# Optimization experiments

Hardware: AMD Instinct MI355X
Metric: run time of the kernel (lower is better)

## Reference

```python
import jax, jax.numpy as jnp
import numpy as np

LN_EPS = 1e-5  # torch.nn.LayerNorm default


def setup_inputs() -> dict:
    key = jax.random.key(0)
    ks = jax.random.split(key, 6)
    b, e, c, h, w, m = 4, 16, 256, 32, 64, 1024
    return {
        "x": jax.random.normal(ks[0], (b, e, c, h, w), dtype=jnp.float32),
        "ln_w": jnp.ones((c, h, w), dtype=jnp.float32),
        "ln_b": jnp.zeros((c, h, w), dtype=jnp.float32),
        "w_in": jax.random.normal(ks[1], (c, m), dtype=jnp.float32) * (1.0 / np.sqrt(c)),
        "b_in": jax.random.normal(ks[2], (m,), dtype=jnp.float32) * 0.01,
        "w_out": jax.random.normal(ks[3], (m, c), dtype=jnp.float32) * (1.0 / np.sqrt(m)),
        "b_out": jax.random.normal(ks[4], (c,), dtype=jnp.float32) * 0.01,
        "gamma": jnp.full((c,), 1e-6, dtype=jnp.float32),
    }


def reference(x, ln_w, ln_b, w_in, b_in, w_out, b_out, gamma):
    # LayerNorm over the last 3 dims (c, h, w) with affine params of shape (c, h, w)
    mu = jnp.mean(x, axis=(-3, -2, -1), keepdims=True)
    var = jnp.var(x, axis=(-3, -2, -1), keepdims=True)  # biased, matches torch
    y = (x - mu) * jax.lax.rsqrt(var + LN_EPS)
    y = y * ln_w + ln_b  # broadcast (c,h,w) over (b,e,...)

    # b e c h w -> b e h w c
    y = jnp.moveaxis(y, 2, -1)
    t = jax.nn.gelu(y @ w_in + b_in, approximate=False)  # torch GELU is exact erf
    t = (t @ w_out + b_out) * gamma  # layer scale on channel dim

    # b e h w c -> b e c h w, residual add
    return x + jnp.moveaxis(t, -1, 2)
```

## Files before the change

### kernel.cpp

```cpp
#include <hip/hip_runtime.h>
#include <math.h>

#define NS 64
#define CD 256
#define HW 2048
#define MD 1024
#define SAMPLE (CD * HW)
#define LN_EPS 1e-5f

#define PB 128
#define MC 32
#define NCH (MD / MC)

typedef float f32x4 __attribute__((ext_vector_type(4)));
typedef long i64;

__device__ __forceinline__ int swz(int p) {
  int k = (p ^ (p >> 2)) & 15;
  return ((k & 7) << 4) | (k & 8);
}

__device__ __forceinline__ void gl_lds16(const unsigned char* g, unsigned char* l) {
  __builtin_amdgcn_global_load_lds(
      (const __attribute__((address_space(1))) unsigned char*)g,
      (__attribute__((address_space(3))) unsigned char*)l, 16, 0, 0);
}

__global__ __launch_bounds__(256) void k_prep(const float* __restrict__ w_in,
                                              const float* __restrict__ w_out,
                                              unsigned char* __restrict__ w_in8p,
                                              unsigned char* __restrict__ w_out8p) {
  int id = blockIdx.x * 256 + threadIdx.x;
  if (id < 65536) {
    int i = id;
    int f = i >> 7, l = (i >> 1) & 63, j0 = (i & 1) * 4;
    int m = (f >> 3) * 16 + (l & 15);
    int c0 = (f & 7) * 32 + (l >> 4) * 8 + j0;
    float a = w_in[(size_t)(c0 + 0) * MD + m];
    float b = w_in[(size_t)(c0 + 1) * MD + m];
    float c = w_in[(size_t)(c0 + 2) * MD + m];
    float d = w_in[(size_t)(c0 + 3) * MD + m];
    int r = __builtin_amdgcn_cvt_pk_fp8_f32(a, b, 0, false);
    r = __builtin_amdgcn_cvt_pk_fp8_f32(c, d, r, true);
    ((int*)w_in8p)[i] = r;
  } else {
    int i = id - 65536;
    int g = i >> 7, l = (i >> 1) & 63, j0 = (i & 1) * 4;
    int c = (g & 15) * 16 + (l & 15);
    int m0 = (g >> 4) * 32 + (l >> 4) * 8 + j0;
    float a = w_out[(size_t)(m0 + 0) * CD + c];
    float b = w_out[(size_t)(m0 + 1) * CD + c];
    float cc = w_out[(size_t)(m0 + 2) * CD + c];
    float d = w_out[(size_t)(m0 + 3) * CD + c];
    int r = __builtin_amdgcn_cvt_pk_fp8_f32(a, b, 0, false);
    r = __builtin_amdgcn_cvt_pk_fp8_f32(cc, d, r, true);
    ((int*)w_out8p)[i] = r;
  }
}

__global__ __launch_bounds__(256) void k_stats1(const float* __restrict__ x,
                                                double* __restrict__ partial) {
  int s = blockIdx.x >> 3, sl = blockIdx.x & 7;
  const float4* p = (const float4*)(x + (size_t)s * SAMPLE + (size_t)sl * 65536);
  double sum = 0.0, ssq = 0.0;
  for (int i = 0; i < 64; ++i) {
    float4 v = p[i * 256 + threadIdx.x];
    sum += (double)v.x + (double)v.y + (double)v.z + (double)v.w;
    ssq += (double)v.x * v.x + (double)v.y * v.y + (double)v.z * v.z + (double)v.w * v.w;
  }
  for (int off = 32; off; off >>= 1) {
    sum += __shfl_down(sum, off);
    ssq += __shfl_down(ssq, off);
  }
  __shared__ double red[4][2];
  int wv = threadIdx.x >> 6, ln = threadIdx.x & 63;
  if (ln == 0) { red[wv][0] = sum; red[wv][1] = ssq; }
  __syncthreads();
  if (threadIdx.x == 0) {
    for (int i = 1; i < 4; ++i) { sum += red[i][0]; ssq += red[i][1]; }
    partial[blockIdx.x * 2] = sum;
    partial[blockIdx.x * 2 + 1] = ssq;
  }
}

__global__ void k_stats2(const double* __restrict__ partial, float* __restrict__ stats) {
  int s = threadIdx.x;
  double sum = 0.0, ssq = 0.0;
  for (int i = 0; i < 8; ++i) {
    sum += partial[(s * 8 + i) * 2];
    ssq += partial[(s * 8 + i) * 2 + 1];
  }
  double mean = sum / (double)SAMPLE;
  double var = ssq / (double)SAMPLE - mean * mean;
  stats[s * 2] = (float)mean;
  stats[s * 2 + 1] = (float)(1.0 / sqrt(var + (double)LN_EPS));
}

__global__ __launch_bounds__(512, 4) void k_fused(
    const float* __restrict__ x, const float* __restrict__ ln_w, const float* __restrict__ ln_b,
    const float* __restrict__ b_in, const float* __restrict__ b_out, const float* __restrict__ gamma,
    const unsigned char* __restrict__ w_in8p, const unsigned char* __restrict__ w_out8p,
    const float* __restrict__ stats, float* __restrict__ out) {
  __shared__ unsigned char Ysh[128 * 256];
  __shared__ unsigned char Wsh1[2][16 * 512];
  __shared__ unsigned char Wsh2[2][16 * 512];

  const int tid = threadIdx.x;
  const int lane = tid & 63, l15 = lane & 15, l4 = lane >> 4;
  const int wv = tid >> 6;
  const int s = blockIdx.x >> 4;
  const int p0 = (blockIdx.x & 15) * PB;
  const float mu = stats[s * 2], rstd = stats[s * 2 + 1];
  const float a_ln = rstd, c_ln = -mu * rstd;
  const size_t xbase = (size_t)s * SAMPLE;

  gl_lds16(w_in8p + wv * 1024 + lane * 16, &Wsh1[0][wv * 1024]);
  gl_lds16(w_out8p + wv * 1024 + lane * 16, &Wsh2[0][wv * 1024]);

  #pragma unroll
  for (int it = 0; it < 4; ++it) {
    int bid = it * 512 + tid;
    int c0 = (bid >> 5) * 4, pp = (bid & 31) * 4;
    float yv[4][4];
    #pragma unroll
    for (int i = 0; i < 4; ++i) {
      size_t off = (size_t)(c0 + i) * HW + p0 + pp;
      float4 xv = *(const float4*)(x + xbase + off);
      float4 lw = *(const float4*)(ln_w + off);
      float4 lb = *(const float4*)(ln_b + off);
      yv[i][0] = fmaf(fmaf(xv.x, a_ln, c_ln), lw.x, lb.x);
      yv[i][1] = fmaf(fmaf(xv.y, a_ln, c_ln), lw.y, lb.y);
      yv[i][2] = fmaf(fmaf(xv.z, a_ln, c_ln), lw.z, lb.z);
      yv[i][3] = fmaf(fmaf(xv.w, a_ln, c_ln), lw.w, lb.w);
    }
    #pragma unroll
    for (int j = 0; j < 4; ++j) {
      int p = pp + j;
      int r = __builtin_amdgcn_cvt_pk_fp8_f32(yv[0][j], yv[1][j], 0, false);
      r = __builtin_amdgcn_cvt_pk_fp8_f32(yv[2][j], yv[3][j], r, true);
      *(int*)&Ysh[p * 256 + (c0 ^ swz(p))] = r;
    }
  }

  const int strip = wv * 16;
  const int pY = strip + l15;
  const int sY = swz(pY);
  f32x4 acc2[16] = {};

  __syncthreads();

  i64 breg[8];
  #pragma unroll
  for (int kk = 0; kk < 8; ++kk)
    breg[kk] = *(const i64*)&Ysh[pY * 256 + ((kk * 32 + l4 * 8) ^ sY)];

  for (int ch = 0; ch < NCH; ++ch) {
    const int b = ch & 1;

    if (ch + 1 < NCH) {
      const size_t co = (size_t)(ch + 1) * 8192;
      gl_lds16(w_in8p + co + wv * 1024 + lane * 16, &Wsh1[b ^ 1][wv * 1024]);
      gl_lds16(w_out8p + co + wv * 1024 + lane * 16, &Wsh2[b ^ 1][wv * 1024]);
    }

    const unsigned char* W1 = Wsh1[b];
    f32x4 acc1[2] = {};
    #pragma unroll
    for (int kk = 0; kk < 8; ++kk) {
      i64 a0 = *(const i64*)&W1[(kk)*512 + lane * 8];
      i64 a1 = *(const i64*)&W1[(8 + kk) * 512 + lane * 8];
      acc1[0] = __builtin_amdgcn_mfma_f32_16x16x32_fp8_fp8(a0, breg[kk], acc1[0], 0, 0, 0);
      acc1[1] = __builtin_amdgcn_mfma_f32_16x16x32_fp8_fp8(a1, breg[kk], acc1[1], 0, 0, 0);
    }

    int pk0, pk1;
    #pragma unroll
    for (int mt = 0; mt < 2; ++mt) {
      const float4 bi = *(const float4*)&b_in[ch * 32 + mt * 16 + l4 * 4];
      float g[4];
      #pragma unroll
      for (int r = 0; r < 4; ++r) {
        float t = acc1[mt][r] + ((const float*)&bi)[r];
        g[r] = t * __builtin_amdgcn_rcpf(1.0f + __expf(-1.702f * t));
      }
      int pk = __builtin_amdgcn_cvt_pk_fp8_f32(g[0], g[1], 0, false);
      pk = __builtin_amdgcn_cvt_pk_fp8_f32(g[2], g[3], pk, true);
      if (mt == 0) pk0 = pk; else pk1 = pk;
    }

    {
      const int sl = l15 + 32 * (l4 & 1);
      int v0a = __shfl(pk0, sl), v0b = __shfl(pk1, sl);
      int v1a = __shfl(pk0, sl + 16), v1b = __shfl(pk1, sl + 16);
      int vlo = (l4 & 2) ? v0b : v0a;
      int vhi = (l4 & 2) ? v1b : v1a;
      i64 a2 = (i64)((((unsigned long long)(unsigned)vhi) << 32) | (unsigned)vlo);

      const unsigned char* W2 = Wsh2[b];
      #pragma unroll
      for (int ct = 0; ct < 16; ++ct) {
        i64 b2 = *(const i64*)&W2[ct * 512 + lane * 8];
        acc2[ct] = __builtin_amdgcn_mfma_f32_16x16x32_fp8_fp8(a2, b2, acc2[ct], 0, 0, 0);
      }
    }

    __syncthreads();
  }

  #pragma unroll
  for (int ct = 0; ct < 16; ++ct) {
    int cc = ct * 16 + l15;
    float gm = gamma[cc], bo = b_out[cc];
    int p = p0 + strip + l4 * 4;
    size_t off = xbase + (size_t)cc * HW + p;
    float4 xv = *(const float4*)(x + off);
    float4 o;
    #pragma unroll
    for (int r = 0; r < 4; ++r)
      ((float*)&o)[r] = ((const float*)&xv)[r] + gm * (acc2[ct][r] + bo);
    *(float4*)(out + off) = o;
  }
}

extern "C" void kernel_launch(void* const* d_in, const int* in_sizes, int n_in,
                              void* d_out, int out_size, void* d_ws, size_t ws_size,
                              hipStream_t stream) {
  const float* x = (const float*)d_in[0];
  const float* ln_w = (const float*)d_in[1];
  const float* ln_b = (const float*)d_in[2];
  const float* w_in = (const float*)d_in[3];
  const float* b_in = (const float*)d_in[4];
  const float* w_out = (const float*)d_in[5];
  const float* b_out = (const float*)d_in[6];
  const float* gamma = (const float*)d_in[7];
  float* out = (float*)d_out;

  char* ws = (char*)d_ws;
  unsigned char* w_in8p = (unsigned char*)ws;
  unsigned char* w_out8p = (unsigned char*)(ws + 262144);
  double* partial = (double*)(ws + 524288);
  float* stats = (float*)(ws + 524288 + 8192);

  k_prep<<<512, 256, 0, stream>>>(w_in, w_out, w_in8p, w_out8p);
  k_stats1<<<512, 256, 0, stream>>>(x, partial);
  k_stats2<<<1, 64, 0, stream>>>(partial, stats);

  k_fused<<<1024, 512, 0, stream>>>(x, ln_w, ln_b, b_in, b_out, gamma,
                                    w_in8p, w_out8p, stats, out);
}
```

Before: 196.0 us.

## Skew second GEMM one chunk behind to overlap GELU with MFMA

Restructures the chunk loop so each iteration runs the second GEMM for the previous chunk's GELU output together with the first GEMM for the current chunk. This gives the scheduler independent MFMA work while GELU, fp8 packing and the lane shuffles are in flight. The w_out staging becomes triple-buffered in dynamic shared memory so the lagging reads stay valid, and s_setprio raises wave priority around the MFMA section. LDS per block grows from 64 KB to 72 KB, and a drain step after the loop handles the last chunk.

```diff
diff --git a/kernel.cpp b/kernel.cpp
--- a/kernel.cpp
+++ b/kernel.cpp
@@ -101,9 +101,10 @@
     const float* __restrict__ b_in, const float* __restrict__ b_out, const float* __restrict__ gamma,
     const unsigned char* __restrict__ w_in8p, const unsigned char* __restrict__ w_out8p,
     const float* __restrict__ stats, float* __restrict__ out) {
-  __shared__ unsigned char Ysh[128 * 256];
-  __shared__ unsigned char Wsh1[2][16 * 512];
-  __shared__ unsigned char Wsh2[2][16 * 512];
+  extern __shared__ unsigned char smem[];
+  unsigned char* Ysh = smem;
+  unsigned char* Wsh1 = smem + 32768;
+  unsigned char* Wsh2 = smem + 49152;
 
   const int tid = threadIdx.x;
   const int lane = tid & 63, l15 = lane & 15, l4 = lane >> 4;
@@ -114,8 +115,8 @@
   const float a_ln = rstd, c_ln = -mu * rstd;
   const size_t xbase = (size_t)s * SAMPLE;
 
-  gl_lds16(w_in8p + wv * 1024 + lane * 16, &Wsh1[0][wv * 1024]);
-  gl_lds16(w_out8p + wv * 1024 + lane * 16, &Wsh2[0][wv * 1024]);
+  gl_lds16(w_in8p + wv * 1024 + lane * 16, Wsh1 + wv * 1024);
+  gl_lds16(w_out8p + wv * 1024 + lane * 16, Wsh2 + wv * 1024);
 
   #pragma unroll
   for (int it = 0; it < 4; ++it) {
@@ -154,16 +155,30 @@
   for (int kk = 0; kk < 8; ++kk)
     breg[kk] = *(const i64*)&Ysh[pY * 256 + ((kk * 32 + l4 * 8) ^ sY)];
 
+  i64 a2_prev = 0;
+
   for (int ch = 0; ch < NCH; ++ch) {
-    const int b = ch & 1;
+    if (ch) __syncthreads();
 
     if (ch + 1 < NCH) {
       const size_t co = (size_t)(ch + 1) * 8192;
-      gl_lds16(w_in8p + co + wv * 1024 + lane * 16, &Wsh1[b ^ 1][wv * 1024]);
-      gl_lds16(w_out8p + co + wv * 1024 + lane * 16, &Wsh2[b ^ 1][wv * 1024]);
-    }
-
-    const unsigned char* W1 = Wsh1[b];
+      gl_lds16(w_in8p + co + wv * 1024 + lane * 16,
+               Wsh1 + ((ch + 1) & 1) * 8192 + wv * 1024);
+      gl_lds16(w_out8p + co + wv * 1024 + lane * 16,
+               Wsh2 + ((ch + 1) % 3) * 8192 + wv * 1024);
+    }
+
+    __builtin_amdgcn_s_setprio(1);
+    if (ch) {
+      const unsigned char* W2 = Wsh2 + ((ch - 1) % 3) * 8192;
+      #pragma unroll
+      for (int ct = 0; ct < 16; ++ct) {
+        i64 b2 = *(const i64*)&W2[ct * 512 + lane * 8];
+        acc2[ct] = __builtin_amdgcn_mfma_f32_16x16x32_fp8_fp8(a2_prev, b2, acc2[ct], 0, 0, 0);
+      }
+    }
+
+    const unsigned char* W1 = Wsh1 + (ch & 1) * 8192;
     f32x4 acc1[2] = {};
     #pragma unroll
     for (int kk = 0; kk < 8; ++kk) {
@@ -172,6 +187,7 @@
       acc1[0] = __builtin_amdgcn_mfma_f32_16x16x32_fp8_fp8(a0, breg[kk], acc1[0], 0, 0, 0);
       acc1[1] = __builtin_amdgcn_mfma_f32_16x16x32_fp8_fp8(a1, breg[kk], acc1[1], 0, 0, 0);
     }
+    __builtin_amdgcn_s_setprio(0);
 
     int pk0, pk1;
     #pragma unroll
@@ -194,17 +210,17 @@
       int v1a = __shfl(pk0, sl + 16), v1b = __shfl(pk1, sl + 16);
       int vlo = (l4 & 2) ? v0b : v0a;
       int vhi = (l4 & 2) ? v1b : v1a;
-      i64 a2 = (i64)((((unsigned long long)(unsigned)vhi) << 32) | (unsigned)vlo);
-
-      const unsigned char* W2 = Wsh2[b];
-      #pragma unroll
-      for (int ct = 0; ct < 16; ++ct) {
-        i64 b2 = *(const i64*)&W2[ct * 512 + lane * 8];
-        acc2[ct] = __builtin_amdgcn_mfma_f32_16x16x32_fp8_fp8(a2, b2, acc2[ct], 0, 0, 0);
-      }
-    }
-
-    __syncthreads();
+      a2_prev = (i64)((((unsigned long long)(unsigned)vhi) << 32) | (unsigned)vlo);
+    }
+  }
+
+  {
+    const unsigned char* W2 = Wsh2 + ((NCH - 1) % 3) * 8192;
+    #pragma unroll
+    for (int ct = 0; ct < 16; ++ct) {
+      i64 b2 = *(const i64*)&W2[ct * 512 + lane * 8];
+      acc2[ct] = __builtin_amdgcn_mfma_f32_16x16x32_fp8_fp8(a2_prev, b2, acc2[ct], 0, 0, 0);
+    }
   }
 
   #pragma unroll
@@ -245,6 +261,9 @@
   k_stats1<<<512, 256, 0, stream>>>(x, partial);
   k_stats2<<<1, 64, 0, stream>>>(partial, stats);
 
-  k_fused<<<1024, 512, 0, stream>>>(x, ln_w, ln_b, b_in, b_out, gamma,
-                                    w_in8p, w_out8p, stats, out);
-}
+  const int lds_bytes = 32768 + 16384 + 24576;
+  hipFuncSetAttribute((const void*)k_fused, hipFuncAttributeMaxDynamicSharedMemorySize,
+                      lds_bytes);
+  k_fused<<<1024, 512, lds_bytes, stream>>>(x, ln_w, ln_b, b_in, b_out, gamma,
+                                            w_in8p, w_out8p, stats, out);
+}
```

After: 182.9 us. 6.7% less time.

## Halve pixel tile, split waves over M/C halves, software-pipeline the two GEMMs

Applied to the files above, without the earlier changes.

The pixel block is halved to 64 and the grid doubled. Pairs of waves now split the hidden chunk and output channels, which halves the accumulator registers and raises the launch-bounds occupancy target. The GELU output is passed through LDS instead of shuffles, and the second GEMM for chunk ch-1 is software-pipelined against the first GEMM for chunk ch. This uses a triple-buffered W_out and s_setprio. The cost is extra barriers per chunk and twice as many reloads of the weights.

```diff
diff --git a/kernel.cpp b/kernel.cpp
--- a/kernel.cpp
+++ b/kernel.cpp
@@ -8,7 +8,7 @@
 #define SAMPLE (CD * HW)
 #define LN_EPS 1e-5f
 
-#define PB 128
+#define PB 64
 #define MC 32
 #define NCH (MD / MC)
 
@@ -96,31 +96,31 @@
   stats[s * 2 + 1] = (float)(1.0 / sqrt(var + (double)LN_EPS));
 }
 
-__global__ __launch_bounds__(512, 4) void k_fused(
+__global__ __launch_bounds__(512, 6) void k_fused(
     const float* __restrict__ x, const float* __restrict__ ln_w, const float* __restrict__ ln_b,
     const float* __restrict__ b_in, const float* __restrict__ b_out, const float* __restrict__ gamma,
     const unsigned char* __restrict__ w_in8p, const unsigned char* __restrict__ w_out8p,
     const float* __restrict__ stats, float* __restrict__ out) {
-  __shared__ unsigned char Ysh[128 * 256];
-  __shared__ unsigned char Wsh1[2][16 * 512];
-  __shared__ unsigned char Wsh2[2][16 * 512];
+  __shared__ unsigned char smem[45056];
+  unsigned char* Ysh = smem + 8192;
 
   const int tid = threadIdx.x;
   const int lane = tid & 63, l15 = lane & 15, l4 = lane >> 4;
   const int wv = tid >> 6;
-  const int s = blockIdx.x >> 4;
-  const int p0 = (blockIdx.x & 15) * PB;
+  const int q = wv >> 1, h = wv & 1;
+  const int s = blockIdx.x >> 5;
+  const int p0 = (blockIdx.x & 31) * PB;
   const float mu = stats[s * 2], rstd = stats[s * 2 + 1];
   const float a_ln = rstd, c_ln = -mu * rstd;
   const size_t xbase = (size_t)s * SAMPLE;
 
-  gl_lds16(w_in8p + wv * 1024 + lane * 16, &Wsh1[0][wv * 1024]);
-  gl_lds16(w_out8p + wv * 1024 + lane * 16, &Wsh2[0][wv * 1024]);
+  gl_lds16(w_in8p + wv * 1024 + lane * 16, smem + 24576 + wv * 1024);
+  gl_lds16(w_out8p + wv * 1024 + lane * 16, smem + wv * 1024);
 
   #pragma unroll
-  for (int it = 0; it < 4; ++it) {
+  for (int it = 0; it < 2; ++it) {
     int bid = it * 512 + tid;
-    int c0 = (bid >> 5) * 4, pp = (bid & 31) * 4;
+    int c0 = (bid >> 4) * 4, pp = (bid & 15) * 4;
     float yv[4][4];
     #pragma unroll
     for (int i = 0; i < 4; ++i) {
@@ -142,10 +142,10 @@
     }
   }
 
-  const int strip = wv * 16;
+  const int strip = q * 16;
   const int pY = strip + l15;
   const int sY = swz(pY);
-  f32x4 acc2[16] = {};
+  f32x4 acc2[8] = {};
 
   __syncthreads();
 
@@ -154,62 +154,69 @@
   for (int kk = 0; kk < 8; ++kk)
     breg[kk] = *(const i64*)&Ysh[pY * 256 + ((kk * 32 + l4 * 8) ^ sY)];
 
+  __syncthreads();
+
   for (int ch = 0; ch < NCH; ++ch) {
-    const int b = ch & 1;
+    if (ch) __syncthreads();
 
     if (ch + 1 < NCH) {
       const size_t co = (size_t)(ch + 1) * 8192;
-      gl_lds16(w_in8p + co + wv * 1024 + lane * 16, &Wsh1[b ^ 1][wv * 1024]);
-      gl_lds16(w_out8p + co + wv * 1024 + lane * 16, &Wsh2[b ^ 1][wv * 1024]);
-    }
-
-    const unsigned char* W1 = Wsh1[b];
-    f32x4 acc1[2] = {};
+      gl_lds16(w_in8p + co + wv * 1024 + lane * 16,
+               smem + 24576 + ((ch + 1) & 1) * 8192 + wv * 1024);
+      gl_lds16(w_out8p + co + wv * 1024 + lane * 16,
+               smem + ((ch + 1) % 3) * 8192 + wv * 1024);
+    }
+
+    __builtin_amdgcn_s_setprio(1);
+    if (ch) {
+      const i64 a2 = *(const i64*)(smem + 40960 + ((ch - 1) & 1) * 2048 +
+                                   q * 512 + l15 * 32 + l4 * 8);
+      const unsigned char* W2 = smem + ((ch - 1) % 3) * 8192;
+      #pragma unroll
+      for (int cti = 0; cti < 8; ++cti) {
+        i64 b2 = *(const i64*)&W2[(h * 8 + cti) * 512 + lane * 8];
+        acc2[cti] = __builtin_amdgcn_mfma_f32_16x16x32_fp8_fp8(a2, b2, acc2[cti], 0, 0, 0);
+      }
+    }
+
+    const unsigned char* W1 = smem + 24576 + (ch & 1) * 8192;
+    f32x4 acc1 = {};
     #pragma unroll
     for (int kk = 0; kk < 8; ++kk) {
-      i64 a0 = *(const i64*)&W1[(kk)*512 + lane * 8];
-      i64 a1 = *(const i64*)&W1[(8 + kk) * 512 + lane * 8];
-      acc1[0] = __builtin_amdgcn_mfma_f32_16x16x32_fp8_fp8(a0, breg[kk], acc1[0], 0, 0, 0);
-      acc1[1] = __builtin_amdgcn_mfma_f32_16x16x32_fp8_fp8(a1, breg[kk], acc1[1], 0, 0, 0);
-    }
-
-    int pk0, pk1;
-    #pragma unroll
-    for (int mt = 0; mt < 2; ++mt) {
-      const float4 bi = *(const float4*)&b_in[ch * 32 + mt * 16 + l4 * 4];
+      i64 a = *(const i64*)&W1[(h * 8 + kk) * 512 + lane * 8];
+      acc1 = __builtin_amdgcn_mfma_f32_16x16x32_fp8_fp8(a, breg[kk], acc1, 0, 0, 0);
+    }
+    __builtin_amdgcn_s_setprio(0);
+
+    {
+      const float4 bi = *(const float4*)&b_in[ch * 32 + h * 16 + l4 * 4];
       float g[4];
       #pragma unroll
       for (int r = 0; r < 4; ++r) {
-        float t = acc1[mt][r] + ((const float*)&bi)[r];
+        float t = acc1[r] + ((const float*)&bi)[r];
         g[r] = t * __builtin_amdgcn_rcpf(1.0f + __expf(-1.702f * t));
       }
       int pk = __builtin_amdgcn_cvt_pk_fp8_f32(g[0], g[1], 0, false);
       pk = __builtin_amdgcn_cvt_pk_fp8_f32(g[2], g[3], pk, true);
-      if (mt == 0) pk0 = pk; else pk1 = pk;
-    }
-
-    {
-      const int sl = l15 + 32 * (l4 & 1);
-      int v0a = __shfl(pk0, sl), v0b = __shfl(pk1, sl);
-      int v1a = __shfl(pk0, sl + 16), v1b = __shfl(pk1, sl + 16);
-      int vlo = (l4 & 2) ? v0b : v0a;
-      int vhi = (l4 & 2) ? v1b : v1a;
-      i64 a2 = (i64)((((unsigned long long)(unsigned)vhi) << 32) | (unsigned)vlo);
-
-      const unsigned char* W2 = Wsh2[b];
-      #pragma unroll
-      for (int ct = 0; ct < 16; ++ct) {
-        i64 b2 = *(const i64*)&W2[ct * 512 + lane * 8];
-        acc2[ct] = __builtin_amdgcn_mfma_f32_16x16x32_fp8_fp8(a2, b2, acc2[ct], 0, 0, 0);
-      }
-    }
-
-    __syncthreads();
+      *(int*)(smem + 40960 + (ch & 1) * 2048 + q * 512 + l15 * 32 + h * 16 + l4 * 4) = pk;
+    }
+  }
+
+  __syncthreads();
+  {
+    const i64 a2 = *(const i64*)(smem + 40960 + ((NCH - 1) & 1) * 2048 +
+                                 q * 512 + l15 * 32 + l4 * 8);
+    const unsigned char* W2 = smem + ((NCH - 1) % 3) * 8192;
+    #pragma unroll
+    for (int cti = 0; cti < 8; ++cti) {
+      i64 b2 = *(const i64*)&W2[(h * 8 + cti) * 512 + lane * 8];
+      acc2[cti] = __builtin_amdgcn_mfma_f32_16x16x32_fp8_fp8(a2, b2, acc2[cti], 0, 0, 0);
+    }
   }
 
   #pragma unroll
-  for (int ct = 0; ct < 16; ++ct) {
-    int cc = ct * 16 + l15;
+  for (int cti = 0; cti < 8; ++cti) {
+    int cc = h * 128 + cti * 16 + l15;
     float gm = gamma[cc], bo = b_out[cc];
     int p = p0 + strip + l4 * 4;
     size_t off = xbase + (size_t)cc * HW + p;
@@ -217,7 +224,7 @@
     float4 o;
     #pragma unroll
     for (int r = 0; r < 4; ++r)
-      ((float*)&o)[r] = ((const float*)&xv)[r] + gm * (acc2[ct][r] + bo);
+      ((float*)&o)[r] = ((const float*)&xv)[r] + gm * (acc2[cti][r] + bo);
     *(float4*)(out + off) = o;
   }
 }
@@ -245,6 +252,6 @@
   k_stats1<<<512, 256, 0, stream>>>(x, partial);
   k_stats2<<<1, 64, 0, stream>>>(partial, stats);
 
-  k_fused<<<1024, 512, 0, stream>>>(x, ln_w, ln_b, b_in, b_out, gamma,
+  k_fused<<<2048, 512, 0, stream>>>(x, ln_w, ln_b, b_in, b_out, gamma,
                                     w_in8p, w_out8p, stats, out);
 }
```

Result: faster. 176.7 us (-9.8%).
